# Kernel tuning notes

Hardware: AMD Instinct MI355X
Metric: run time of the kernel (lower is better)

## Reference

```python
import jax, jax.numpy as jnp
import numpy as np
import math

# Model dims (see shape_source)
BATCH, SEQ, HH, WW = 32, 128, 32, 32   # x: (B, seq_len, H, W); L = H*W = 1024
D_MODEL = 1024                          # hidden_dim
N2 = 4                                  # n=8 -> 4 complex S4D modes
L_MAX = 64                              # SSM kernel length (l_max)


def _layernorm(x, gamma, beta, eps=1e-5):
    mu = jnp.mean(x, axis=-1, keepdims=True)
    var = jnp.var(x, axis=-1, keepdims=True)
    return (x - mu) * jax.lax.rsqrt(var + eps) * gamma + beta


def setup_inputs() -> dict:
    key = jax.random.key(0)
    ks = jax.random.split(key, 12)
    d_in = SEQ  # d_input = d_output = seq_len
    inp = {
        "x": jax.random.normal(ks[0], (BATCH, SEQ, HH, WW), dtype=jnp.float32),
        # encoder Linear(d_input -> d_model)
        "W_enc": jax.random.normal(ks[1], (d_in, D_MODEL), dtype=jnp.float32) / math.sqrt(d_in),
        "b_enc": jnp.zeros((D_MODEL,), dtype=jnp.float32),
        # S4D SSM parameters (per d_model channel, N2 complex modes)
        "log_dt": (jax.random.uniform(ks[2], (D_MODEL,), dtype=jnp.float32)
                   * (math.log(0.1) - math.log(0.001)) + math.log(0.001)),
        "A_log_real": jnp.full((D_MODEL, N2), math.log(0.5), dtype=jnp.float32),
        "A_imag": jnp.broadcast_to(math.pi * jnp.arange(N2, dtype=jnp.float32), (D_MODEL, N2)).copy(),
        "C_real": jax.random.normal(ks[3], (D_MODEL, N2), dtype=jnp.float32) * 0.5,
        "C_imag": jax.random.normal(ks[4], (D_MODEL, N2), dtype=jnp.float32) * 0.5,
        "D": jax.random.normal(ks[5], (D_MODEL,), dtype=jnp.float32),
        # position-wise GLU mixing Linear(d_model -> 2*d_model)
        "W_glu": jax.random.normal(ks[6], (D_MODEL, 2 * D_MODEL), dtype=jnp.float32) / math.sqrt(D_MODEL),
        "b_glu": jnp.zeros((2 * D_MODEL,), dtype=jnp.float32),
        "ln_gamma": jnp.ones((D_MODEL,), dtype=jnp.float32),
        "ln_beta": jnp.zeros((D_MODEL,), dtype=jnp.float32),
        # decoder Linear(d_model -> d_output)
        "W_dec": jax.random.normal(ks[7], (D_MODEL, d_in), dtype=jnp.float32) / math.sqrt(D_MODEL),
        "b_dec": jnp.zeros((d_in,), dtype=jnp.float32),
    }
    return inp


def reference(x, W_enc, b_enc, log_dt, A_log_real, A_imag, C_real, C_imag, D,
              W_glu, b_glu, ln_gamma, ln_beta, W_dec, b_dec):
    Bsz, S, Hh, Ww = x.shape
    L = Hh * Ww
    u = x.reshape(Bsz, S, L)                                  # (B, d_input, L)
    # encoder applied per position along L
    h = jnp.einsum('bdl,de->ble', u, W_enc) + b_enc           # (B, L, d_model)

    # ---- S4D kernel (ZOH discretization, B=1, diagonal A) ----
    dt = jnp.exp(log_dt)                                      # (d,)
    A = -jnp.exp(A_log_real) + 1j * A_imag                    # (d, n2) complex
    Cc = C_real + 1j * C_imag
    dtA = A * dt[:, None]                                     # (d, n2)
    Bd = (jnp.exp(dtA) - 1.0) / A                             # ZOH input matrix
    t = jnp.arange(L_MAX)
    vand = jnp.exp(dtA[:, :, None] * t)                       # (d, n2, l_max)
    K = 2.0 * jnp.einsum('dn,dnl->dl', Cc * Bd, vand).real    # (d, l_max)

    # ---- causal FFT convolution along L + skip D*u ----
    z = jnp.swapaxes(h, 1, 2)                                 # (B, d, L)
    n_fft = L + L_MAX
    y = jnp.fft.irfft(jnp.fft.rfft(z, n=n_fft) * jnp.fft.rfft(K, n=n_fft), n=n_fft)[..., :L]
    y = y + D[:, None] * z                                    # (B, d, L)

    # ---- block: GELU -> GLU mixing -> residual -> LayerNorm ----
    y = jax.nn.gelu(jnp.swapaxes(y, 1, 2))                    # (B, L, d)
    g = y @ W_glu + b_glu                                     # (B, L, 2d)
    g = g[..., :D_MODEL] * jax.nn.sigmoid(g[..., D_MODEL:])
    h = _layernorm(h + g, ln_gamma, ln_beta)                  # (B, L, d)

    out = h @ W_dec + b_dec                                   # (B, L, d_output)
    out = jnp.swapaxes(out, 1, 2).reshape(Bsz, S, Hh, Ww)
    return out
```

## Files before the change

### kernel.cpp

```cpp
#include <hip/hip_runtime.h>
#include <hip/hip_bf16.h>
#include <math.h>

#define B_ 32
#define S_ 128
#define L_ 1024
#define D_ 1024

typedef unsigned short u16;
typedef __attribute__((ext_vector_type(8))) __bf16 bf16x8;
typedef __attribute__((ext_vector_type(4))) float f32x4;

__device__ __forceinline__ float bf2f(u16 u) {
    return __uint_as_float(((unsigned)u) << 16);
}
__device__ __forceinline__ u16 f2bf(float f) {
    unsigned u = __float_as_uint(f);
    u += 0x7FFF + ((u >> 16) & 1);
    return (u16)(u >> 16);
}
__device__ __forceinline__ float gelu_tanh(float x) {
    float x3 = x * x * x;
    float t = tanhf(0.7978845608028654f * (x + 0.044715f * x3));
    return 0.5f * x * (1.0f + t);
}
__device__ __forceinline__ float sigmoidf(float x) {
    return 1.0f / (1.0f + expf(-x));
}
__device__ __forceinline__ void gld16(const void* g, void* l) {
    __builtin_amdgcn_global_load_lds((const __attribute__((address_space(1))) void*)g,
                                     (__attribute__((address_space(3))) void*)l, 16, 0, 0);
}

__global__ __launch_bounds__(256) void k_ssmk(
        const float* __restrict__ log_dt, const float* __restrict__ Alr,
        const float* __restrict__ Aim, const float* __restrict__ Cr,
        const float* __restrict__ Ci, float* __restrict__ Kt) {
    int tid = blockIdx.x * 256 + threadIdx.x;
    int d = tid & (D_ - 1);
    int j = tid >> 10;
    float dt = expf(log_dt[d]);
    float acc = 0.f;
    #pragma unroll
    for (int n = 0; n < 4; ++n) {
        float ar = -expf(Alr[d * 4 + n]);
        float ai = Aim[d * 4 + n];
        float wr = ar * dt, wi = ai * dt;
        float ew = expf(wr);
        float sw, cw; sincosf(wi, &sw, &cw);
        float ur = ew * cw - 1.0f, ui = ew * sw;
        float inv = 1.0f / (ar * ar + ai * ai);
        float bdr = (ur * ar + ui * ai) * inv;
        float bdi = (ui * ar - ur * ai) * inv;
        float cr = Cr[d * 4 + n], ci = Ci[d * 4 + n];
        float cbr = cr * bdr - ci * bdi;
        float cbi = cr * bdi + ci * bdr;
        float ej = expf(wr * (float)j);
        float sj, cj; sincosf(wi * (float)j, &sj, &cj);
        acc += 2.0f * ej * (cbr * cj - cbi * sj);
    }
    Kt[j * D_ + d] = acc;
}

__global__ __launch_bounds__(256) void k_tcast(
        const float* __restrict__ src0, u16* __restrict__ dst0, int R, int C) {
    __shared__ float tile[64][65];
    const float* src = src0 + (size_t)blockIdx.z * R * C;
    u16* dst = dst0 + (size_t)blockIdx.z * R * C;
    int c0 = blockIdx.x * 64;
    int r0 = blockIdx.y * 64;
    int t = threadIdx.x;
    #pragma unroll
    for (int p = 0; p < 4; ++p) {
        int fid = p * 256 + t;
        int rr = fid >> 4, cc = (fid & 15) * 4;
        float4 v = *(const float4*)&src[(size_t)(r0 + rr) * C + c0 + cc];
        tile[rr][cc + 0] = v.x; tile[rr][cc + 1] = v.y;
        tile[rr][cc + 2] = v.z; tile[rr][cc + 3] = v.w;
    }
    __syncthreads();
    #pragma unroll
    for (int p = 0; p < 4; ++p) {
        int fid = p * 256 + t;
        int rr = fid >> 4, cc = (fid & 15) * 4;
        ushort4 o;
        o.x = f2bf(tile[cc + 0][rr]);
        o.y = f2bf(tile[cc + 1][rr]);
        o.z = f2bf(tile[cc + 2][rr]);
        o.w = f2bf(tile[cc + 3][rr]);
        *(ushort4*)&dst[(size_t)(c0 + rr) * R + r0 + cc] = o;
    }
}

__global__ __launch_bounds__(256) void k_enc_mfma(
        const u16* __restrict__ xb, const u16* __restrict__ WeT,
        const float* __restrict__ be, u16* __restrict__ hb) {
    __shared__ u16 As[128 * 128];
    __shared__ u16 Bs[128 * 128];
    int t = threadIdx.x;
    int lane = t & 63, wid = t >> 6;
    int wr = wid & 1, wc = wid >> 1;
    int orig = blockIdx.x;
    int wgid = (orig & 7) * 256 + (orig >> 3);
    int m0 = (wgid >> 3) * 128;
    int e0 = (wgid & 7) * 128;

    #pragma unroll
    for (int c = 0; c < 8; ++c) {
        int ch = wid * 8 + c;
        int r = ch * 4 + (lane >> 4);
        int g = (lane & 15) ^ (r & 15);
        gld16(&xb[(size_t)(m0 + r) * 128 + g * 8], &As[ch * 512]);
        gld16(&WeT[(size_t)(e0 + r) * 128 + g * 8], &Bs[ch * 512]);
    }
    int co4[4];
    #pragma unroll
    for (int kh = 0; kh < 4; ++kh)
        co4[kh] = ((((lane >> 4) + kh * 4) ^ (lane & 15)) * 8);
    int arow[4], brow[4];
    #pragma unroll
    for (int i = 0; i < 4; ++i) arow[i] = (wr * 64 + i * 16 + (lane & 15)) * 128;
    #pragma unroll
    for (int q = 0; q < 4; ++q) brow[q] = (wc * 64 + q * 16 + (lane & 15)) * 128;

    __syncthreads();
    f32x4 acc[4][4] = {};
    #pragma unroll
    for (int kh = 0; kh < 4; ++kh) {
        bf16x8 af[4], bfr[4];
        #pragma unroll
        for (int i = 0; i < 4; ++i) af[i] = *(const bf16x8*)&As[arow[i] + co4[kh]];
        #pragma unroll
        for (int q = 0; q < 4; ++q) bfr[q] = *(const bf16x8*)&Bs[brow[q] + co4[kh]];
        __builtin_amdgcn_s_setprio(1);
        #pragma unroll
        for (int i = 0; i < 4; ++i)
            #pragma unroll
            for (int q = 0; q < 4; ++q)
                acc[i][q] = __builtin_amdgcn_mfma_f32_16x16x32_bf16(af[i], bfr[q], acc[i][q], 0, 0, 0);
        __builtin_amdgcn_s_setprio(0);
    }
    #pragma unroll
    for (int q = 0; q < 4; ++q) {
        int e = e0 + wc * 64 + q * 16 + (lane & 15);
        float bias = be[e];
        #pragma unroll
        for (int i = 0; i < 4; ++i) {
            #pragma unroll
            for (int r = 0; r < 4; ++r) {
                int m = m0 + wr * 64 + i * 16 + (lane >> 4) * 4 + r;
                hb[(size_t)m * 1024 + e] = f2bf(acc[i][q][r] + bias);
            }
        }
    }
}

__global__ __launch_bounds__(256) void k_conv(
        const u16* __restrict__ hb, const float* __restrict__ Kt,
        const float* __restrict__ Dv, u16* __restrict__ yg) {
    __shared__ float hs[128][64];
    int b = blockIdx.z;
    int l0 = blockIdx.y * 64;
    int d0 = blockIdx.x * 64;
    int t = threadIdx.x;
    int dl = t & 63, lg = t >> 6;
    #pragma unroll
    for (int p = 0; p < 8; ++p) {
        int fid = p * 256 + t;
        int r = fid >> 4, c4 = fid & 15;
        int l = l0 - 64 + r;
        float4 v = make_float4(0.f, 0.f, 0.f, 0.f);
        if (l >= 0) {
            ushort4 u = *(const ushort4*)&hb[((size_t)b * 1024 + l) * 1024 + d0 + c4 * 4];
            v = make_float4(bf2f(u.x), bf2f(u.y), bf2f(u.z), bf2f(u.w));
        }
        *(float4*)&hs[r][c4 * 4] = v;
    }
    float kr[64];
    #pragma unroll
    for (int j = 0; j < 64; ++j) kr[j] = Kt[j * 1024 + d0 + dl];
    float Dd = Dv[d0 + dl];
    __syncthreads();
    float acc[16] = {};
    int rbase = lg * 16 + 1;
    #pragma unroll
    for (int s = 0; s < 15; ++s) {
        float hv = hs[rbase + s][dl];
        #pragma unroll
        for (int i = 0; i <= 14; ++i)
            if (i <= s) acc[i] = fmaf(kr[i + 63 - s], hv, acc[i]);
    }
    #pragma unroll
    for (int s = 15; s < 64; ++s) {
        float hv = hs[rbase + s][dl];
        #pragma unroll
        for (int i = 0; i < 16; ++i)
            acc[i] = fmaf(kr[i + 63 - s], hv, acc[i]);
    }
    #pragma unroll
    for (int s = 64; s < 79; ++s) {
        float hv = hs[rbase + s][dl];
        #pragma unroll
        for (int i = 1; i < 16; ++i)
            if (i >= s - 63) acc[i] = fmaf(kr[i + 63 - s], hv, acc[i]);
    }
    #pragma unroll
    for (int i = 0; i < 16; ++i) {
        int l = l0 + lg * 16 + i;
        float z = hs[64 + lg * 16 + i][dl];
        float y = acc[i] + Dd * z;
        yg[((size_t)b * 1024 + l) * 1024 + d0 + dl] = f2bf(gelu_tanh(y));
    }
}

__global__ __launch_bounds__(512, 2) void k_glu256(
        const u16* __restrict__ yg, const u16* __restrict__ WgT,
        const float* __restrict__ bg, u16* __restrict__ hb) {
    __shared__ u16 S[65536];
    int t = threadIdx.x;
    int lane = t & 63, wid = t >> 6;
    int wr = wid >> 2, wc = wid & 3;

    int orig = blockIdx.x;
    int wgid = (orig & 7) * 128 + (orig >> 3);
    int m0 = (wgid >> 3) * 256;
    int p0g = (wgid & 7) * 128;

    int gofs = (((lane & 7) ^ ((lane >> 3) & 7)) * 8);
    int ch0 = wid * 2, ch1 = ch0 + 1;
    int dst0 = ch0 * 512 + lane * 8;
    int dst1 = ch1 * 512 + lane * 8;
    int gmA[2][2], gmB[2][2];
    #pragma unroll
    for (int h = 0; h < 2; ++h) {
        #pragma unroll
        for (int j = 0; j < 2; ++j) {
            int ch = ch0 + j;
            gmA[h][j] = m0 + (ch >> 3) * 128 + h * 64 + (ch & 7) * 8 + (lane >> 3);
            int r = (ch >> 2) * 64 + h * 32 + (ch & 3) * 8 + (lane >> 3);
            gmB[h][j] = ((r >> 4) & 1) * 1024 + p0g + (((r >> 5) << 4) | (r & 15));
        }
    }
    int co[2];
    co[0] = (((lane >> 4) + 0) ^ (lane & 7)) * 8;
    co[1] = (((lane >> 4) + 4) ^ (lane & 7)) * 8;
    int arow[4], brow[2];
    #pragma unroll
    for (int i = 0; i < 4; ++i) arow[i] = (wr * 64 + i * 16 + (lane & 15)) * 64;
    #pragma unroll
    for (int q = 0; q < 2; ++q) brow[q] = (wc * 32 + q * 16 + (lane & 15)) * 64;

#define GLD_A(H, BUF, K0) { u16* d_ = &S[((BUF) * 2 + (H)) * 8192]; \
    gld16(&yg[(size_t)gmA[H][0] * 1024 + (K0) + gofs], d_ + dst0); \
    gld16(&yg[(size_t)gmA[H][1] * 1024 + (K0) + gofs], d_ + dst1); }
#define GLD_B(H, BUF, K0) { u16* d_ = &S[32768 + ((BUF) * 2 + (H)) * 8192]; \
    gld16(&WgT[(size_t)gmB[H][0] * 1024 + (K0) + gofs], d_ + dst0); \
    gld16(&WgT[(size_t)gmB[H][1] * 1024 + (K0) + gofs], d_ + dst1); }

#define RD_AH(MS) { const u16* Ar_ = &S[(cbuf * 2 + (MS)) * 8192]; \
    _Pragma("unroll") for (int i = 0; i < 4; ++i) { \
        a_[i][0] = *(const bf16x8*)&Ar_[arow[i] + co[0]]; \
        a_[i][1] = *(const bf16x8*)&Ar_[arow[i] + co[1]]; } }
#define RD_BH(NS, BB) { const u16* Br_ = &S[32768 + (cbuf * 2 + (NS)) * 8192]; \
    _Pragma("unroll") for (int q = 0; q < 2; ++q) { \
        BB[q][0] = *(const bf16x8*)&Br_[brow[q] + co[0]]; \
        BB[q][1] = *(const bf16x8*)&Br_[brow[q] + co[1]]; } }
#define MFMA16(MS, NS, BB) { __builtin_amdgcn_s_setprio(1); \
    _Pragma("unroll") for (int i = 0; i < 4; ++i) \
        _Pragma("unroll") for (int q = 0; q < 2; ++q) { \
            acc[(MS) * 4 + i][(NS) * 2 + q] = __builtin_amdgcn_mfma_f32_16x16x32_bf16( \
                a_[i][0], BB[q][0], acc[(MS) * 4 + i][(NS) * 2 + q], 0, 0, 0); \
            acc[(MS) * 4 + i][(NS) * 2 + q] = __builtin_amdgcn_mfma_f32_16x16x32_bf16( \
                a_[i][1], BB[q][1], acc[(MS) * 4 + i][(NS) * 2 + q], 0, 0, 0); } \
    __builtin_amdgcn_s_setprio(0); }
#define BAR() { __builtin_amdgcn_s_barrier(); __builtin_amdgcn_sched_barrier(0); }

    f32x4 acc[8][4] = {};
    bf16x8 a_[4][2], b0_[2][2], b1_[2][2];

    GLD_A(0, 0, 0); GLD_B(0, 0, 0); GLD_B(1, 0, 0); GLD_A(1, 0, 0);
    GLD_A(0, 1, 64); GLD_B(0, 1, 64);

    for (int kt = 0; kt < 15; ++kt) {
        int cbuf = kt & 1, nbuf = cbuf ^ 1;
        int k1 = (kt + 1) * 64, k2 = (kt + 2) * 64;
        asm volatile("s_waitcnt vmcnt(4)" ::: "memory");
        BAR();
        RD_BH(0, b0_); RD_BH(1, b1_); RD_AH(0);
        GLD_B(1, nbuf, k1);
        MFMA16(0, 0, b0_);
        BAR();
        GLD_A(1, nbuf, k1);
        MFMA16(0, 1, b1_);
        BAR();
        RD_AH(1);
        if (kt < 14) GLD_A(0, cbuf, k2);
        MFMA16(1, 0, b0_);
        BAR();
        if (kt < 14) GLD_B(0, cbuf, k2);
        MFMA16(1, 1, b1_);
    }
    {
        int cbuf = 1;
        asm volatile("s_waitcnt vmcnt(0)" ::: "memory");
        BAR();
        RD_BH(0, b0_); RD_BH(1, b1_); RD_AH(0);
        MFMA16(0, 0, b0_);
        MFMA16(0, 1, b1_);
        RD_AH(1);
        MFMA16(1, 0, b0_);
        MFMA16(1, 1, b1_);
    }
#undef GLD_A
#undef GLD_B
#undef RD_AH
#undef RD_BH
#undef MFMA16
#undef BAR

    #pragma unroll
    for (int i = 0; i < 8; ++i) {
        #pragma unroll
        for (int pb = 0; pb < 2; ++pb) {
            int col = p0g + (wc * 2 + pb) * 16 + (lane & 15);
            float b1v = bg[col];
            float b2v = bg[1024 + col];
            #pragma unroll
            for (int r = 0; r < 4; ++r) {
                int m = m0 + wr * 128 + i * 16 + (lane >> 4) * 4 + r;
                size_t idx = (size_t)m * 1024 + col;
                float g1 = acc[i][pb * 2][r] + b1v;
                float g2 = acc[i][pb * 2 + 1][r] + b2v;
                hb[idx] = f2bf(bf2f(hb[idx]) + g1 * sigmoidf(g2));
            }
        }
    }
}

__global__ __launch_bounds__(256) void k_ln(
        u16* __restrict__ hb, const float* __restrict__ gamma,
        const float* __restrict__ beta) {
    int row = blockIdx.x;
    int t = threadIdx.x;
    size_t base = (size_t)row * 1024;
    ushort4 u = *(const ushort4*)&hb[base + t * 4];
    float v0 = bf2f(u.x), v1 = bf2f(u.y), v2 = bf2f(u.z), v3 = bf2f(u.w);
    float s = v0 + v1 + v2 + v3;
    float s2 = v0 * v0 + v1 * v1 + v2 * v2 + v3 * v3;
    #pragma unroll
    for (int off = 32; off > 0; off >>= 1) {
        s += __shfl_down(s, off);
        s2 += __shfl_down(s2, off);
    }
    __shared__ float rs[4], rs2[4];
    int wid = t >> 6, lane = t & 63;
    if (lane == 0) { rs[wid] = s; rs2[wid] = s2; }
    __syncthreads();
    float ts = rs[0] + rs[1] + rs[2] + rs[3];
    float ts2 = rs2[0] + rs2[1] + rs2[2] + rs2[3];
    float mean = ts * (1.0f / 1024.0f);
    float var = ts2 * (1.0f / 1024.0f) - mean * mean;
    float rstd = rsqrtf(var + 1e-5f);
    float4 gm = *(const float4*)&gamma[t * 4];
    float4 bt = *(const float4*)&beta[t * 4];
    ushort4 o;
    o.x = f2bf((v0 - mean) * rstd * gm.x + bt.x);
    o.y = f2bf((v1 - mean) * rstd * gm.y + bt.y);
    o.z = f2bf((v2 - mean) * rstd * gm.z + bt.z);
    o.w = f2bf((v3 - mean) * rstd * gm.w + bt.w);
    *(ushort4*)&hb[base + t * 4] = o;
}

__global__ __launch_bounds__(256) void k_dec_mfma(
        const u16* __restrict__ hb, const u16* __restrict__ WdT,
        const float* __restrict__ bd, float* __restrict__ out) {
    __shared__ __align__(16) char smem[65536];
    u16* As = (u16*)smem;
    u16* Bs = (u16*)(smem + 32768);
    float* Ts = (float*)smem;
    int t = threadIdx.x;
    int lane = t & 63, wid = t >> 6;
    int wr = wid & 1, wc = wid >> 1;
    int m0 = blockIdx.x * 128;
    int bb = m0 >> 10, l0 = m0 & 1023;

    int gsrc = (((lane & 7) ^ (lane >> 3)) * 8);
    int rr4[4];
    #pragma unroll
    for (int c = 0; c < 4; ++c) rr4[c] = (wid * 4 + c) * 8 + (lane >> 3);
    int co[2];
    co[0] = (((lane >> 4) + 0) ^ (lane & 7)) * 8;
    co[1] = (((lane >> 4) + 4) ^ (lane & 7)) * 8;
    int arow[4], brow[4];
    #pragma unroll
    for (int i = 0; i < 4; ++i) arow[i] = (wr * 64 + i * 16 + (lane & 15)) * 64;
    #pragma unroll
    for (int q = 0; q < 4; ++q) brow[q] = (wc * 64 + q * 16 + (lane & 15)) * 64;

    f32x4 acc[4][4] = {};
    #pragma unroll
    for (int c = 0; c < 4; ++c) {
        int ch = wid * 4 + c;
        gld16(&hb[(size_t)(m0 + rr4[c]) * 1024 + gsrc], &As[0 * 8192 + ch * 512]);
        gld16(&WdT[(size_t)rr4[c] * 1024 + gsrc], &Bs[0 * 8192 + ch * 512]);
    }
    __syncthreads();
    int cur = 0;
    for (int kt = 0; kt < 16; ++kt) {
        if (kt < 15) {
            int k0 = (kt + 1) * 64;
            #pragma unroll
            for (int c = 0; c < 4; ++c) {
                int ch = wid * 4 + c;
                gld16(&hb[(size_t)(m0 + rr4[c]) * 1024 + k0 + gsrc], &As[(cur ^ 1) * 8192 + ch * 512]);
                gld16(&WdT[(size_t)rr4[c] * 1024 + k0 + gsrc], &Bs[(cur ^ 1) * 8192 + ch * 512]);
            }
        }
        #pragma unroll
        for (int kh = 0; kh < 2; ++kh) {
            bf16x8 af[4], bfr[4];
            #pragma unroll
            for (int i = 0; i < 4; ++i) af[i] = *(const bf16x8*)&As[cur * 8192 + arow[i] + co[kh]];
            #pragma unroll
            for (int q = 0; q < 4; ++q) bfr[q] = *(const bf16x8*)&Bs[cur * 8192 + brow[q] + co[kh]];
            __builtin_amdgcn_s_setprio(1);
            #pragma unroll
            for (int i = 0; i < 4; ++i)
                #pragma unroll
                for (int q = 0; q < 4; ++q)
                    acc[i][q] = __builtin_amdgcn_mfma_f32_16x16x32_bf16(af[i], bfr[q], acc[i][q], 0, 0, 0);
            __builtin_amdgcn_s_setprio(0);
        }
        __syncthreads();
        cur ^= 1;
    }
    __syncthreads();
    #pragma unroll
    for (int ro = 0; ro < 2; ++ro) {
        if (wc == ro) {
            #pragma unroll
            for (int i = 0; i < 4; ++i)
                #pragma unroll
                for (int q = 0; q < 4; ++q) {
                    int sl = q * 16 + (lane & 15);
                    float bias = bd[ro * 64 + sl];
                    #pragma unroll
                    for (int r = 0; r < 4; ++r) {
                        int ml = wr * 64 + i * 16 + (lane >> 4) * 4 + r;
                        Ts[sl * 132 + ml] = acc[i][q][r] + bias;
                    }
                }
        }
        __syncthreads();
        #pragma unroll
        for (int p = 0; p < 8; ++p) {
            int fid = p * 256 + t;
            int sl = fid >> 5, c = (fid & 31) * 4;
            float4 v = *(const float4*)&Ts[sl * 132 + c];
            *(float4*)&out[(size_t)bb * 131072 + (size_t)(ro * 64 + sl) * 1024 + l0 + c] = v;
        }
        __syncthreads();
    }
}

extern "C" void kernel_launch(void* const* d_in, const int* in_sizes, int n_in,
                              void* d_out, int out_size, void* d_ws, size_t ws_size,
                              hipStream_t stream) {
    (void)in_sizes; (void)n_in; (void)out_size; (void)ws_size;
    const float* x   = (const float*)d_in[0];
    const float* We  = (const float*)d_in[1];
    const float* be  = (const float*)d_in[2];
    const float* ldt = (const float*)d_in[3];
    const float* Alr = (const float*)d_in[4];
    const float* Aim = (const float*)d_in[5];
    const float* Cr  = (const float*)d_in[6];
    const float* Ci  = (const float*)d_in[7];
    const float* Dv  = (const float*)d_in[8];
    const float* Wg  = (const float*)d_in[9];
    const float* bg  = (const float*)d_in[10];
    const float* gam = (const float*)d_in[11];
    const float* bet = (const float*)d_in[12];
    const float* Wd  = (const float*)d_in[13];
    const float* bd  = (const float*)d_in[14];
    float* out = (float*)d_out;

    u16* hb = (u16*)d_ws;
    u16* yg = hb + 33554432ull;
    float* Kt = (float*)(yg + 33554432ull);
    u16* WgT = (u16*)(Kt + 65536);
    u16* WdT = WgT + 2097152ull;
    u16* WeT = WdT + 131072ull;
    u16* xb  = yg;

    k_tcast<<<dim3(32, 16, 1), 256, 0, stream>>>(Wg, WgT, 1024, 2048);
    k_tcast<<<dim3(2, 16, 1), 256, 0, stream>>>(Wd, WdT, 1024, 128);
    k_tcast<<<dim3(16, 2, 1), 256, 0, stream>>>(We, WeT, 128, 1024);
    k_tcast<<<dim3(16, 2, 32), 256, 0, stream>>>(x, xb, 128, 1024);
    k_ssmk<<<256, 256, 0, stream>>>(ldt, Alr, Aim, Cr, Ci, Kt);
    k_enc_mfma<<<2048, 256, 0, stream>>>(xb, WeT, be, hb);
    k_conv<<<dim3(16, 16, 32), 256, 0, stream>>>(hb, Kt, Dv, yg);
    k_glu256<<<1024, 512, 0, stream>>>(yg, WgT, bg, hb);
    k_ln<<<32768, 256, 0, stream>>>(hb, gam, bet);
    k_dec_mfma<<<256, 256, 0, stream>>>(hb, WdT, bd, out);
}
```

Before: 343.0 us.

## Fold LayerNorm into GLU epilogue and decoder via row statistics

```diff
diff --git a/kernel.cpp b/kernel.cpp
--- a/kernel.cpp
+++ b/kernel.cpp
@@ -62,8 +62,43 @@
     Kt[j * D_ + d] = acc;
 }
 
+__global__ __launch_bounds__(256) void k_zero(float* __restrict__ p) {
+    int tid = blockIdx.x * 256 + threadIdx.x;
+    *(float4*)&p[tid * 4] = make_float4(0.f, 0.f, 0.f, 0.f);
+}
+
+__global__ __launch_bounds__(256) void k_c12(
+        const float* __restrict__ Wd, const float* __restrict__ gam,
+        const float* __restrict__ bet, const float* __restrict__ bd,
+        float* __restrict__ c12) {
+    int s = blockIdx.x;
+    int t = threadIdx.x;
+    float a1 = 0.f, a2 = 0.f;
+    #pragma unroll
+    for (int it = 0; it < 4; ++it) {
+        int k = it * 256 + t;
+        float w = Wd[(size_t)k * 128 + s];
+        a1 += gam[k] * w;
+        a2 += bet[k] * w;
+    }
+    #pragma unroll
+    for (int off = 32; off > 0; off >>= 1) {
+        a1 += __shfl_down(a1, off);
+        a2 += __shfl_down(a2, off);
+    }
+    __shared__ float r1[4], r2[4];
+    int wid = t >> 6, lane = t & 63;
+    if (lane == 0) { r1[wid] = a1; r2[wid] = a2; }
+    __syncthreads();
+    if (t == 0) {
+        c12[s] = r1[0] + r1[1] + r1[2] + r1[3];
+        c12[128 + s] = r2[0] + r2[1] + r2[2] + r2[3] + bd[s];
+    }
+}
+
 __global__ __launch_bounds__(256) void k_tcast(
-        const float* __restrict__ src0, u16* __restrict__ dst0, int R, int C) {
+        const float* __restrict__ src0, u16* __restrict__ dst0, int R, int C,
+        const float* __restrict__ rowscale) {
     __shared__ float tile[64][65];
     const float* src = src0 + (size_t)blockIdx.z * R * C;
     u16* dst = dst0 + (size_t)blockIdx.z * R * C;
@@ -75,8 +110,9 @@
         int fid = p * 256 + t;
         int rr = fid >> 4, cc = (fid & 15) * 4;
         float4 v = *(const float4*)&src[(size_t)(r0 + rr) * C + c0 + cc];
-        tile[rr][cc + 0] = v.x; tile[rr][cc + 1] = v.y;
-        tile[rr][cc + 2] = v.z; tile[rr][cc + 3] = v.w;
+        float sc = rowscale ? rowscale[r0 + rr] : 1.0f;
+        tile[rr][cc + 0] = v.x * sc; tile[rr][cc + 1] = v.y * sc;
+        tile[rr][cc + 2] = v.z * sc; tile[rr][cc + 3] = v.w * sc;
     }
     __syncthreads();
     #pragma unroll
@@ -215,8 +251,9 @@
 
 __global__ __launch_bounds__(512, 2) void k_glu256(
         const u16* __restrict__ yg, const u16* __restrict__ WgT,
-        const float* __restrict__ bg, u16* __restrict__ hb) {
-    __shared__ u16 S[65536];
+        const float* __restrict__ bg, u16* __restrict__ hb,
+        float* __restrict__ rowS) {
+    __shared__ __align__(16) u16 S[65536];
     int t = threadIdx.x;
     int lane = t & 63, wid = t >> 6;
     int wr = wid >> 2, wc = wid & 3;
@@ -318,72 +355,83 @@
 #undef MFMA16
 #undef BAR
 
-    #pragma unroll
-    for (int i = 0; i < 8; ++i) {
-        #pragma unroll
-        for (int pb = 0; pb < 2; ++pb) {
-            int col = p0g + (wc * 2 + pb) * 16 + (lane & 15);
-            float b1v = bg[col];
-            float b2v = bg[1024 + col];
-            #pragma unroll
-            for (int r = 0; r < 4; ++r) {
-                int m = m0 + wr * 128 + i * 16 + (lane >> 4) * 4 + r;
-                size_t idx = (size_t)m * 1024 + col;
-                float g1 = acc[i][pb * 2][r] + b1v;
-                float g2 = acc[i][pb * 2 + 1][r] + b2v;
-                hb[idx] = f2bf(bf2f(hb[idx]) + g1 * sigmoidf(g2));
+    float* Ts = (float*)S;
+    int erow = t >> 3;
+    int ecg = (t & 7) * 16;
+    #pragma unroll
+    for (int chunk = 0; chunk < 4; ++chunk) {
+        __syncthreads();
+        if (wr == (chunk >> 1)) {
+            #pragma unroll
+            for (int ii = 0; ii < 4; ++ii) {
+                int i = (chunk & 1) * 4 + ii;
+                #pragma unroll
+                for (int pb = 0; pb < 2; ++pb) {
+                    int col = (wc * 2 + pb) * 16 + (lane & 15);
+                    float b1v = bg[p0g + col];
+                    float b2v = bg[1024 + p0g + col];
+                    #pragma unroll
+                    for (int r = 0; r < 4; ++r) {
+                        int rloc = ii * 16 + (lane >> 4) * 4 + r;
+                        float g1 = acc[i][pb * 2][r] + b1v;
+                        float g2 = acc[i][pb * 2 + 1][r] + b2v;
+                        Ts[rloc * 132 + col] = g1 * sigmoidf(g2);
+                    }
+                }
             }
         }
-    }
-}
-
-__global__ __launch_bounds__(256) void k_ln(
-        u16* __restrict__ hb, const float* __restrict__ gamma,
-        const float* __restrict__ beta) {
-    int row = blockIdx.x;
-    int t = threadIdx.x;
-    size_t base = (size_t)row * 1024;
-    ushort4 u = *(const ushort4*)&hb[base + t * 4];
-    float v0 = bf2f(u.x), v1 = bf2f(u.y), v2 = bf2f(u.z), v3 = bf2f(u.w);
-    float s = v0 + v1 + v2 + v3;
-    float s2 = v0 * v0 + v1 * v1 + v2 * v2 + v3 * v3;
-    #pragma unroll
-    for (int off = 32; off > 0; off >>= 1) {
-        s += __shfl_down(s, off);
-        s2 += __shfl_down(s2, off);
-    }
-    __shared__ float rs[4], rs2[4];
-    int wid = t >> 6, lane = t & 63;
-    if (lane == 0) { rs[wid] = s; rs2[wid] = s2; }
-    __syncthreads();
-    float ts = rs[0] + rs[1] + rs[2] + rs[3];
-    float ts2 = rs2[0] + rs2[1] + rs2[2] + rs2[3];
-    float mean = ts * (1.0f / 1024.0f);
-    float var = ts2 * (1.0f / 1024.0f) - mean * mean;
-    float rstd = rsqrtf(var + 1e-5f);
-    float4 gm = *(const float4*)&gamma[t * 4];
-    float4 bt = *(const float4*)&beta[t * 4];
-    ushort4 o;
-    o.x = f2bf((v0 - mean) * rstd * gm.x + bt.x);
-    o.y = f2bf((v1 - mean) * rstd * gm.y + bt.y);
-    o.z = f2bf((v2 - mean) * rstd * gm.z + bt.z);
-    o.w = f2bf((v3 - mean) * rstd * gm.w + bt.w);
-    *(ushort4*)&hb[base + t * 4] = o;
+        __syncthreads();
+        int gm = m0 + chunk * 64 + erow;
+        size_t gbase = (size_t)gm * 1024 + p0g + ecg;
+        float rs1 = 0.f, rs2 = 0.f;
+        #pragma unroll
+        for (int h = 0; h < 2; ++h) {
+            uint4 hv = *(uint4*)&hb[gbase + h * 8];
+            u16* hu = (u16*)&hv;
+            #pragma unroll
+            for (int e = 0; e < 8; ++e) {
+                float v = bf2f(hu[e]) + Ts[erow * 132 + ecg + h * 8 + e];
+                rs1 += v;
+                rs2 += v * v;
+                hu[e] = f2bf(v);
+            }
+            *(uint4*)&hb[gbase + h * 8] = hv;
+        }
+        rs1 += __shfl_xor(rs1, 1); rs2 += __shfl_xor(rs2, 1);
+        rs1 += __shfl_xor(rs1, 2); rs2 += __shfl_xor(rs2, 2);
+        rs1 += __shfl_xor(rs1, 4); rs2 += __shfl_xor(rs2, 4);
+        if ((lane & 7) == 0) {
+            atomicAdd(&rowS[gm], rs1);
+            atomicAdd(&rowS[32768 + gm], rs2);
+        }
+    }
 }
 
 __global__ __launch_bounds__(256) void k_dec_mfma(
         const u16* __restrict__ hb, const u16* __restrict__ WdT,
-        const float* __restrict__ bd, float* __restrict__ out) {
-    __shared__ __align__(16) char smem[65536];
+        const float* __restrict__ rowS, const float* __restrict__ c12,
+        float* __restrict__ out) {
+    __shared__ __align__(16) char smem[66560];
     u16* As = (u16*)smem;
     u16* Bs = (u16*)(smem + 32768);
     float* Ts = (float*)smem;
+    float* muL = (float*)(smem + 65536);
+    float* rsL = (float*)(smem + 65536 + 512);
     int t = threadIdx.x;
     int lane = t & 63, wid = t >> 6;
     int wr = wid & 1, wc = wid >> 1;
     int m0 = blockIdx.x * 128;
     int bb = m0 >> 10, l0 = m0 & 1023;
 
+    if (t < 128) {
+        float s1 = rowS[m0 + t];
+        float s2 = rowS[32768 + m0 + t];
+        float mu = s1 * (1.0f / 1024.0f);
+        float var = s2 * (1.0f / 1024.0f) - mu * mu;
+        muL[t] = mu;
+        rsL[t] = rsqrtf(var + 1e-5f);
+    }
+
     int gsrc = (((lane & 7) ^ (lane >> 3)) * 8);
     int rr4[4];
     #pragma unroll
@@ -443,11 +491,13 @@
                 #pragma unroll
                 for (int q = 0; q < 4; ++q) {
                     int sl = q * 16 + (lane & 15);
-                    float bias = bd[ro * 64 + sl];
+                    float c1v = c12[ro * 64 + sl];
+                    float c2v = c12[128 + ro * 64 + sl];
                     #pragma unroll
                     for (int r = 0; r < 4; ++r) {
                         int ml = wr * 64 + i * 16 + (lane >> 4) * 4 + r;
-                        Ts[sl * 132 + ml] = acc[i][q][r] + bias;
+                        float rst = rsL[ml];
+                        Ts[sl * 132 + ml] = rst * acc[i][q][r] - muL[ml] * rst * c1v + c2v;
                     }
                 }
         }
@@ -491,15 +541,18 @@
     u16* WdT = WgT + 2097152ull;
     u16* WeT = WdT + 131072ull;
     u16* xb  = yg;
-
-    k_tcast<<<dim3(32, 16, 1), 256, 0, stream>>>(Wg, WgT, 1024, 2048);
-    k_tcast<<<dim3(2, 16, 1), 256, 0, stream>>>(Wd, WdT, 1024, 128);
-    k_tcast<<<dim3(16, 2, 1), 256, 0, stream>>>(We, WeT, 128, 1024);
-    k_tcast<<<dim3(16, 2, 32), 256, 0, stream>>>(x, xb, 128, 1024);
+    float* rowS = Kt;
+    float* c12  = (float*)WeT;
+
+    k_tcast<<<dim3(32, 16, 1), 256, 0, stream>>>(Wg, WgT, 1024, 2048, nullptr);
+    k_tcast<<<dim3(2, 16, 1), 256, 0, stream>>>(Wd, WdT, 1024, 128, gam);
+    k_tcast<<<dim3(16, 2, 1), 256, 0, stream>>>(We, WeT, 128, 1024, nullptr);
+    k_tcast<<<dim3(16, 2, 32), 256, 0, stream>>>(x, xb, 128, 1024, nullptr);
     k_ssmk<<<256, 256, 0, stream>>>(ldt, Alr, Aim, Cr, Ci, Kt);
     k_enc_mfma<<<2048, 256, 0, stream>>>(xb, WeT, be, hb);
     k_conv<<<dim3(16, 16, 32), 256, 0, stream>>>(hb, Kt, Dv, yg);
-    k_glu256<<<1024, 512, 0, stream>>>(yg, WgT, bg, hb);
-    k_ln<<<32768, 256, 0, stream>>>(hb, gam, bet);
-    k_dec_mfma<<<256, 256, 0, stream>>>(hb, WdT, bd, out);
-}
+    k_c12<<<128, 256, 0, stream>>>(Wd, gam, bet, bd, c12);
+    k_zero<<<64, 256, 0, stream>>>(rowS);
+    k_glu256<<<1024, 512, 0, stream>>>(yg, WgT, bg, hb, rowS);
+    k_dec_mfma<<<256, 256, 0, stream>>>(hb, WdT, rowS, c12, out);
+}
```

Result: faster. 336.2 us (-2.0%).
